# Kernel optimization log

Measured on AMD Instinct MI355X. Metric: run time of the kernel, lower is better.

## Reference

```python
import jax, jax.numpy as jnp
import numpy as np
import math

GOLDEN_CENTER = 1.0 / math.e
GOLDEN_LOWER = 0.5 - math.log(4.0 / 3.0)
GOLDEN_UPPER = 0.5

B, T, D = 4, 2048, 1024
E = 8
I = 4096 // (E // 2)  # expert_inter = 1024


def setup_inputs() -> dict:
    key = jax.random.key(0)
    k = jax.random.split(key, 6)
    s_d = 1.0 / math.sqrt(D)
    s_i = 1.0 / math.sqrt(I)
    return {
        "x": jax.random.normal(k[0], (B, T, D), jnp.float32),
        "Wg": jax.random.normal(k[1], (E, D, I), jnp.float32) * s_d,
        "Wu": jax.random.normal(k[2], (E, D, I), jnp.float32) * s_d,
        "Wd": jax.random.normal(k[3], (E, I, D), jnp.float32) * s_i,
        "Wr": jax.random.normal(k[4], (D, E), jnp.float32) * s_d,
        "temperature": jnp.ones((1,), jnp.float32),
    }


def _routing_weights(x, Wr, temperature):
    # inhibition: [B,T,E]
    inh = jax.nn.sigmoid((x @ Wr) / temperature)
    in_zone = (inh >= GOLDEN_LOWER) & (inh <= GOLDEN_UPPER)
    dist = jnp.abs(inh - GOLDEN_CENTER)
    w = jnp.exp(-dist / 0.1) * in_zone.astype(x.dtype)
    wsum = w.sum(axis=-1, keepdims=True)
    no_expert = wsum < 1e-8
    # fallback: softer decay, keep top-2 experts, renormalize
    fb = jnp.exp(-dist / 0.3)
    _, top2 = jax.lax.top_k(fb, 2)  # [B,T,2]
    fb_mask = jax.nn.one_hot(top2, E, dtype=x.dtype).sum(axis=-2)  # [B,T,E]
    fb_w = fb * fb_mask
    fb_w = fb_w / jnp.clip(fb_w.sum(axis=-1, keepdims=True), 1e-8)
    w = jnp.where(no_expert, fb_w, w)
    wsum = w.sum(axis=-1, keepdims=True)
    return w / jnp.clip(wsum, 1e-8)


def reference(x, Wg, Wu, Wd, Wr, temperature):
    weights = _routing_weights(x, Wr, temperature)  # [B,T,E]
    gate = jnp.einsum("btd,edi->beti", x, Wg)
    up = jnp.einsum("btd,edi->beti", x, Wu)
    h = jax.nn.silu(gate) * up  # [B,E,T,I]
    e_out = jnp.einsum("beti,eid->betd", h, Wd)
    out = jnp.einsum("bte,betd->btd", weights, e_out)
    return out
```

## Files before the change

kernel.cpp:

```cpp
#include <hip/hip_runtime.h>
#include <hip/hip_bf16.h>
#include <cstdint>

typedef __attribute__((ext_vector_type(8))) _Float16 f16x8;
typedef __attribute__((ext_vector_type(4))) _Float16 f16x4;
typedef __attribute__((ext_vector_type(4))) float f32x4;

#define GOLDEN_CENTER_F 0.36787944117144233f
#define GOLDEN_LOWER_F  0.21231792754821915f
#define GOLDEN_UPPER_F  0.5f

static constexpr int Dm = 1024;
static constexpr int Im = 1024;
static constexpr int NTOK = 8192;
static constexpr int NE = 8;

__device__ __forceinline__ void async16(const _Float16* g, _Float16* l) {
  __builtin_amdgcn_global_load_lds(
      (const __attribute__((address_space(1))) void*)g,
      (__attribute__((address_space(3))) void*)l,
      16, 0, 0);
}

__global__ void routing_kernel(const float* __restrict__ x, const float* __restrict__ Wr,
                               const float* __restrict__ temp, float* __restrict__ wts) {
  const int wave = threadIdx.x >> 6, lane = threadIdx.x & 63;
  const int t = blockIdx.x * 4 + wave;
  const float* xr = x + (size_t)t * Dm;
  float acc[NE] = {0.f,0.f,0.f,0.f,0.f,0.f,0.f,0.f};
  for (int d = lane; d < Dm; d += 64) {
    float xv = xr[d];
    const float* wr = Wr + (size_t)d * NE;
#pragma unroll
    for (int e = 0; e < NE; ++e) acc[e] += xv * wr[e];
  }
#pragma unroll
  for (int off = 32; off > 0; off >>= 1) {
#pragma unroll
    for (int e = 0; e < NE; ++e) acc[e] += __shfl_down(acc[e], off, 64);
  }
  if (lane == 0) {
    float T = temp[0];
    float w[NE], dist[NE];
    float wsum = 0.f;
#pragma unroll
    for (int e = 0; e < NE; ++e) {
      float inh = 1.f / (1.f + expf(-acc[e] / T));
      dist[e] = fabsf(inh - GOLDEN_CENTER_F);
      bool zone = (inh >= GOLDEN_LOWER_F) && (inh <= GOLDEN_UPPER_F);
      w[e] = zone ? expf(-dist[e] / 0.1f) : 0.f;
      wsum += w[e];
    }
    if (wsum < 1e-8f) {
      float fb[NE];
#pragma unroll
      for (int e = 0; e < NE; ++e) fb[e] = expf(-dist[e] / 0.3f);
      int i1 = 0;
      for (int e = 1; e < NE; ++e) if (fb[e] > fb[i1]) i1 = e;
      int i2 = (i1 == 0) ? 1 : 0;
      for (int e = 0; e < NE; ++e) if (e != i1 && fb[e] > fb[i2]) i2 = e;
      float s = fmaxf(fb[i1] + fb[i2], 1e-8f);
#pragma unroll
      for (int e = 0; e < NE; ++e) w[e] = 0.f;
      w[i1] = fb[i1] / s;
      w[i2] = fb[i2] / s;
      wsum = w[i1] + w[i2];
    }
    float inv = 1.f / fmaxf(wsum, 1e-8f);
#pragma unroll
    for (int e = 0; e < NE; ++e) wts[(size_t)t * NE + e] = w[e] * inv;
  }
}

__global__ void compact_kernel(const float* __restrict__ wts, int* __restrict__ tok,
                               float* __restrict__ wc, int* __restrict__ cnt,
                               int* __restrict__ pos) {
  const int e = blockIdx.x;
  const int tid = threadIdx.x;
  const int wave = tid >> 6, lane = tid & 63;
  __shared__ int wcnt[4];
  __shared__ int s_running;
  if (tid == 0) s_running = 0;
  __syncthreads();
  for (int base = 0; base < NTOK; base += 256) {
    int t = base + tid;
    float w = wts[(size_t)t * NE + e];
    bool act = w > 0.f;
    unsigned long long mask = __ballot(act);
    int prefix = __popcll(mask & ((1ull << lane) - 1ull));
    if (lane == 0) wcnt[wave] = __popcll(mask);
    __syncthreads();
    int wbase = 0;
    for (int i = 0; i < wave; ++i) wbase += wcnt[i];
    int run = s_running;
    int p = run + wbase + prefix;
    pos[(size_t)t * NE + e] = act ? p : -1;
    if (act) {
      tok[(size_t)e * NTOK + p] = t;
      wc[(size_t)e * NTOK + p] = w;
    }
    __syncthreads();
    if (tid == 0) s_running = run + wcnt[0] + wcnt[1] + wcnt[2] + wcnt[3];
    __syncthreads();
  }
  int c = s_running;
  if (tid == 0) cnt[e] = c;
  int padded = (c + 127) & ~127;
  for (int p = c + tid; p < padded; p += 256) {
    tok[(size_t)e * NTOK + p] = 0;
    wc[(size_t)e * NTOK + p] = 0.f;
  }
}

__global__ void cvt_x_kernel(const float* __restrict__ x, _Float16* __restrict__ xb) {
  size_t i = ((size_t)blockIdx.x * 256 + threadIdx.x) * 4;
  float4 v = *(const float4*)(x + i);
  f16x4 o = {(_Float16)v.x, (_Float16)v.y, (_Float16)v.z, (_Float16)v.w};
  *(f16x4*)(xb + i) = o;
}

__global__ void transpose_cvt_kernel(const float* __restrict__ Wg, const float* __restrict__ Wu,
                                     const float* __restrict__ Wd, _Float16* __restrict__ WgT,
                                     _Float16* __restrict__ WuT, _Float16* __restrict__ WdT) {
  __shared__ float tile[32][33];
  const int which = blockIdx.z >> 3;
  const int e = blockIdx.z & 7;
  const float* src = which == 0 ? Wg : which == 1 ? Wu : Wd;
  _Float16* dst = which == 0 ? WgT : which == 1 ? WuT : WdT;
  const size_t base = (size_t)e * 1024 * 1024;
  const int r0 = blockIdx.y * 32, c0 = blockIdx.x * 32;
  const int tx = threadIdx.x & 31, ty = threadIdx.x >> 5;
#pragma unroll
  for (int j = 0; j < 32; j += 8)
    tile[ty + j][tx] = src[base + (size_t)(r0 + ty + j) * 1024 + c0 + tx];
  __syncthreads();
#pragma unroll
  for (int j = 0; j < 32; j += 8)
    dst[base + (size_t)(c0 + ty + j) * 1024 + r0 + tx] = (_Float16)tile[tx][ty + j];
}

__global__ __launch_bounds__(256, 2) void gemm1_kernel(
    const _Float16* __restrict__ A, const _Float16* __restrict__ BgAll,
    const _Float16* __restrict__ BuAll, const int* __restrict__ tok,
    const int* __restrict__ cnt, _Float16* __restrict__ hbuf, int ebase) {
  constexpr int K = Dm;
  const int z = blockIdx.z;
  const int e = ebase + z;
  const int r0 = blockIdx.x * 128;
  if (r0 >= cnt[e]) return;
  const int n0 = blockIdx.y * 128;
  const _Float16* Bg = BgAll + (size_t)e * Dm * Im;
  const _Float16* Bu = BuAll + (size_t)e * Dm * Im;
  _Float16* H = hbuf + (size_t)z * NTOK * Im;
  const int* tk = tok + (size_t)e * NTOK;

  __shared__ _Float16 As[128 * 32];
  __shared__ _Float16 Bgs[128 * 32];
  __shared__ _Float16 Bus[128 * 32];
  const int tid = threadIdx.x;
  const int wave = tid >> 6, lane = tid & 63;
  const int m_off = (wave & 1) * 64, n_off = (wave >> 1) * 64;

  f32x4 accg[4][4], accu[4][4];
#pragma unroll
  for (int i = 0; i < 4; ++i)
#pragma unroll
    for (int j = 0; j < 4; ++j) { accg[i][j] = (f32x4)0.f; accu[i][j] = (f32x4)0.f; }

  const int srow = lane >> 2;
  const int scol = ((lane & 3) ^ ((srow >> 1) & 3)) * 8;
  const int ridx = r0 + wave * 32 + srow;
  const int tA0 = tk[ridx];
  const int tA1 = tk[ridx + 16];
  const _Float16* gA0 = A + (size_t)tA0 * K + scol;
  const _Float16* gA1 = A + (size_t)tA1 * K + scol;
  const _Float16* gBg = Bg + (size_t)(n0 + wave * 32 + srow) * K + scol;
  const _Float16* gBu = Bu + (size_t)(n0 + wave * 32 + srow) * K + scol;
  _Float16* lA  = As  + (wave * 32) * 32;
  _Float16* lBg = Bgs + (wave * 32) * 32;
  _Float16* lBu = Bus + (wave * 32) * 32;

  const int fr = lane & 15, fq = lane >> 4;
  const int sw = (fq ^ ((fr >> 1) & 3)) * 8;
  const int aoff = (m_off + fr) * 32 + sw;
  const int boff = (n_off + fr) * 32 + sw;

  for (int k0 = 0; k0 < K; k0 += 32) {
    __syncthreads();
    async16(gA0 + k0, lA);
    async16(gA1 + k0, lA + 16 * 32);
    async16(gBg + k0, lBg);
    async16(gBg + k0 + 16 * K, lBg + 16 * 32);
    async16(gBu + k0, lBu);
    async16(gBu + k0 + 16 * K, lBu + 16 * 32);
    __syncthreads();

    f16x8 af[4], bgf[4], buf2[4];
#pragma unroll
    for (int i = 0; i < 4; ++i) {
      af[i]   = *(const f16x8*)(As  + aoff + i * 16 * 32);
      bgf[i]  = *(const f16x8*)(Bgs + boff + i * 16 * 32);
      buf2[i] = *(const f16x8*)(Bus + boff + i * 16 * 32);
    }
#pragma unroll
    for (int im = 0; im < 4; ++im)
#pragma unroll
      for (int in2 = 0; in2 < 4; ++in2) {
        accg[im][in2] = __builtin_amdgcn_mfma_f32_16x16x32_f16(af[im], bgf[in2], accg[im][in2], 0, 0, 0);
        accu[im][in2] = __builtin_amdgcn_mfma_f32_16x16x32_f16(af[im], buf2[in2], accu[im][in2], 0, 0, 0);
      }
  }

#pragma unroll
  for (int im = 0; im < 4; ++im)
#pragma unroll
    for (int in2 = 0; in2 < 4; ++in2)
#pragma unroll
      for (int r = 0; r < 4; ++r) {
        int row = r0 + m_off + im * 16 + fq * 4 + r;
        int c = n0 + n_off + in2 * 16 + fr;
        float g = accg[im][in2][r], u = accu[im][in2][r];
        float s = g / (1.f + __expf(-g));
        H[(size_t)row * Im + c] = (_Float16)(s * u);
      }
}

__global__ __launch_bounds__(256, 2) void gemm2_kernel(
    const _Float16* __restrict__ hbuf, const _Float16* __restrict__ BAll,
    const int* __restrict__ cnt, _Float16* __restrict__ ebuf, int ebase) {
  constexpr int K = Im;
  const int z = blockIdx.z;
  const int e = ebase + z;
  const int r0 = blockIdx.x * 128;
  if (r0 >= cnt[e]) return;
  const int n0 = blockIdx.y * 128;
  const _Float16* A = hbuf + (size_t)z * NTOK * Im;
  const _Float16* B = BAll + (size_t)e * Im * Dm;
  _Float16* Ez = ebuf + (size_t)z * NTOK * Dm;

  __shared__ _Float16 As[128 * 32];
  __shared__ _Float16 Bs[128 * 32];
  const int tid = threadIdx.x;
  const int wave = tid >> 6, lane = tid & 63;
  const int m_off = (wave & 1) * 64, n_off = (wave >> 1) * 64;

  f32x4 acc[4][4];
#pragma unroll
  for (int i = 0; i < 4; ++i)
#pragma unroll
    for (int j = 0; j < 4; ++j) acc[i][j] = (f32x4)0.f;

  const int srow = lane >> 2;
  const int scol = ((lane & 3) ^ ((srow >> 1) & 3)) * 8;
  const _Float16* gA = A + (size_t)(r0 + wave * 32 + srow) * K + scol;
  const _Float16* gB = B + (size_t)(n0 + wave * 32 + srow) * K + scol;
  _Float16* lA = As + (wave * 32) * 32;
  _Float16* lB = Bs + (wave * 32) * 32;

  const int fr = lane & 15, fq = lane >> 4;
  const int sw = (fq ^ ((fr >> 1) & 3)) * 8;
  const int aoff = (m_off + fr) * 32 + sw;
  const int boff = (n_off + fr) * 32 + sw;

  for (int k0 = 0; k0 < K; k0 += 32) {
    __syncthreads();
    async16(gA + k0, lA);
    async16(gA + k0 + 16 * K, lA + 16 * 32);
    async16(gB + k0, lB);
    async16(gB + k0 + 16 * K, lB + 16 * 32);
    __syncthreads();

    f16x8 af[4], bf[4];
#pragma unroll
    for (int i = 0; i < 4; ++i) {
      af[i] = *(const f16x8*)(As + aoff + i * 16 * 32);
      bf[i] = *(const f16x8*)(Bs + boff + i * 16 * 32);
    }
#pragma unroll
    for (int im = 0; im < 4; ++im)
#pragma unroll
      for (int in2 = 0; in2 < 4; ++in2)
        acc[im][in2] = __builtin_amdgcn_mfma_f32_16x16x32_f16(af[im], bf[in2], acc[im][in2], 0, 0, 0);
  }

#pragma unroll
  for (int im = 0; im < 4; ++im)
#pragma unroll
    for (int in2 = 0; in2 < 4; ++in2)
#pragma unroll
      for (int r = 0; r < 4; ++r) {
        int row = m_off + im * 16 + fq * 4 + r;
        int c = n0 + n_off + in2 * 16 + fr;
        Ez[((size_t)(r0 + row)) * Dm + c] = (_Float16)acc[im][in2][r];
      }
}

__global__ void combine_kernel(const _Float16* __restrict__ ebuf, const int* __restrict__ pos,
                               const float* __restrict__ wts, float* __restrict__ out,
                               int ebase, int g, int accum) {
  const int t = blockIdx.x;
  __shared__ int sp[NE];
  __shared__ float sw[NE];
  if (threadIdx.x < g) {
    sp[threadIdx.x] = pos[(size_t)t * NE + ebase + threadIdx.x];
    sw[threadIdx.x] = wts[(size_t)t * NE + ebase + threadIdx.x];
  }
  __syncthreads();
  const int c = threadIdx.x * 4;
  float4 s;
  if (accum) s = *(const float4*)(out + (size_t)t * Dm + c);
  else s = float4{0.f, 0.f, 0.f, 0.f};
  for (int j = 0; j < g; ++j) {
    int p = sp[j];
    if (p >= 0) {
      float w = sw[j];
      f16x4 v = *(const f16x4*)(ebuf + ((size_t)j * NTOK + p) * Dm + c);
      s.x += w * (float)v[0];
      s.y += w * (float)v[1];
      s.z += w * (float)v[2];
      s.w += w * (float)v[3];
    }
  }
  *(float4*)(out + (size_t)t * Dm + c) = s;
}

extern "C" void kernel_launch(void* const* d_in, const int* in_sizes, int n_in,
                              void* d_out, int out_size, void* d_ws, size_t ws_size,
                              hipStream_t stream) {
  const float* x    = (const float*)d_in[0];
  const float* Wg   = (const float*)d_in[1];
  const float* Wu   = (const float*)d_in[2];
  const float* Wd   = (const float*)d_in[3];
  const float* Wr   = (const float*)d_in[4];
  const float* temp = (const float*)d_in[5];
  float* out = (float*)d_out;

  char* ws = (char*)d_ws;
  size_t off = 0;
  auto carve = [&](size_t bytes) {
    char* p = ws + off;
    off = (off + bytes + 255) & ~(size_t)255;
    return p;
  };
  float* wts = (float*)carve((size_t)NTOK * NE * 4);
  int*   tok = (int*)  carve((size_t)NE * NTOK * 4);
  float* wc  = (float*)carve((size_t)NE * NTOK * 4);
  int*   pos = (int*)  carve((size_t)NTOK * NE * 4);
  int*   cnt = (int*)  carve(4096);
  _Float16* xb   = (_Float16*)carve((size_t)NTOK * Dm * 2);
  _Float16* WgT  = (_Float16*)carve((size_t)NE * Dm * Im * 2);
  _Float16* WuT  = (_Float16*)carve((size_t)NE * Dm * Im * 2);
  _Float16* WdT  = (_Float16*)carve((size_t)NE * Dm * Im * 2);
  const size_t fixed_off = off;
  const size_t per_expert = (size_t)NTOK * Im * 2 + (size_t)NTOK * Dm * 2;
  int g = (ws_size >= fixed_off + 8 * per_expert) ? 8 : 4;
  _Float16* hbuf = (_Float16*)carve((size_t)g * NTOK * Im * 2);
  _Float16* ebuf = (_Float16*)carve((size_t)g * NTOK * Dm * 2);

  routing_kernel<<<NTOK / 4, 256, 0, stream>>>(x, Wr, temp, wts);
  compact_kernel<<<NE, 256, 0, stream>>>(wts, tok, wc, cnt, pos);
  cvt_x_kernel<<<(NTOK * Dm) / 1024, 256, 0, stream>>>(x, xb);
  transpose_cvt_kernel<<<dim3(32, 32, 24), 256, 0, stream>>>(Wg, Wu, Wd, WgT, WuT, WdT);

  for (int e0 = 0; e0 < NE; e0 += g) {
    gemm1_kernel<<<dim3(NTOK / 128, Im / 128, g), 256, 0, stream>>>(xb, WgT, WuT, tok, cnt, hbuf, e0);
    gemm2_kernel<<<dim3(NTOK / 128, Dm / 128, g), 256, 0, stream>>>(hbuf, WdT, cnt, ebuf, e0);
    combine_kernel<<<NTOK, 256, 0, stream>>>(ebuf, pos, wts, out, e0, g, e0 > 0);
  }
}
```

Baseline: 487.7 us.

## Double-buffer GEMM K-loop with 64-wide tiles and interleave gate/up weights

Both expert GEMMs now use double-buffered LDS tiles of K=64, issuing async loads for the next tile before computing the current one and waiting with explicit vmcnt counters instead of two full barriers per step. Gate and up weights are packed into one interleaved [2048 x D] matrix so gemm1 runs as a single GEMM whose adjacent 16-column blocks pair gate and up for the SiLU epilogue. The fp16 conversion of x is folded into the routing kernel, removing a separate launch and a second read of x. LDS use per block rises to 64KB, which may limit occupancy.

```diff
diff --git a/kernel.cpp b/kernel.cpp
--- a/kernel.cpp
+++ b/kernel.cpp
@@ -23,16 +23,23 @@
 }
 
 __global__ void routing_kernel(const float* __restrict__ x, const float* __restrict__ Wr,
-                               const float* __restrict__ temp, float* __restrict__ wts) {
+                               const float* __restrict__ temp, float* __restrict__ wts,
+                               _Float16* __restrict__ xb) {
   const int wave = threadIdx.x >> 6, lane = threadIdx.x & 63;
   const int t = blockIdx.x * 4 + wave;
   const float* xr = x + (size_t)t * Dm;
+  _Float16* xo = xb + (size_t)t * Dm;
   float acc[NE] = {0.f,0.f,0.f,0.f,0.f,0.f,0.f,0.f};
-  for (int d = lane; d < Dm; d += 64) {
-    float xv = xr[d];
-    const float* wr = Wr + (size_t)d * NE;
-#pragma unroll
-    for (int e = 0; e < NE; ++e) acc[e] += xv * wr[e];
+  const int d0 = lane * 16;
+#pragma unroll
+  for (int j = 0; j < 4; ++j) {
+    float4 v = *(const float4*)(xr + d0 + j * 4);
+    f16x4 h = {(_Float16)v.x, (_Float16)v.y, (_Float16)v.z, (_Float16)v.w};
+    *(f16x4*)(xo + d0 + j * 4) = h;
+    const float* wr = Wr + (size_t)(d0 + j * 4) * NE;
+#pragma unroll
+    for (int e = 0; e < NE; ++e)
+      acc[e] += v.x * wr[e] + v.y * wr[NE + e] + v.z * wr[2 * NE + e] + v.w * wr[3 * NE + e];
   }
 #pragma unroll
   for (int off = 32; off > 0; off >>= 1) {
@@ -112,137 +119,170 @@
   }
 }
 
-__global__ void cvt_x_kernel(const float* __restrict__ x, _Float16* __restrict__ xb) {
-  size_t i = ((size_t)blockIdx.x * 256 + threadIdx.x) * 4;
-  float4 v = *(const float4*)(x + i);
-  f16x4 o = {(_Float16)v.x, (_Float16)v.y, (_Float16)v.z, (_Float16)v.w};
-  *(f16x4*)(xb + i) = o;
-}
-
 __global__ void transpose_cvt_kernel(const float* __restrict__ Wg, const float* __restrict__ Wu,
-                                     const float* __restrict__ Wd, _Float16* __restrict__ WgT,
-                                     _Float16* __restrict__ WuT, _Float16* __restrict__ WdT) {
+                                     const float* __restrict__ Wd, _Float16* __restrict__ Wgu,
+                                     _Float16* __restrict__ WdT) {
   __shared__ float tile[32][33];
   const int which = blockIdx.z >> 3;
   const int e = blockIdx.z & 7;
   const float* src = which == 0 ? Wg : which == 1 ? Wu : Wd;
-  _Float16* dst = which == 0 ? WgT : which == 1 ? WuT : WdT;
-  const size_t base = (size_t)e * 1024 * 1024;
+  const size_t sbase = (size_t)e * 1024 * 1024;
   const int r0 = blockIdx.y * 32, c0 = blockIdx.x * 32;
   const int tx = threadIdx.x & 31, ty = threadIdx.x >> 5;
 #pragma unroll
   for (int j = 0; j < 32; j += 8)
-    tile[ty + j][tx] = src[base + (size_t)(r0 + ty + j) * 1024 + c0 + tx];
+    tile[ty + j][tx] = src[sbase + (size_t)(r0 + ty + j) * 1024 + c0 + tx];
   __syncthreads();
 #pragma unroll
-  for (int j = 0; j < 32; j += 8)
-    dst[base + (size_t)(c0 + ty + j) * 1024 + r0 + tx] = (_Float16)tile[tx][ty + j];
-}
+  for (int j = 0; j < 32; j += 8) {
+    const int c = c0 + ty + j;
+    float v = tile[tx][ty + j];
+    if (which == 2) {
+      WdT[sbase + (size_t)c * 1024 + r0 + tx] = (_Float16)v;
+    } else {
+      const int n = ((c >> 4) << 5) + (which << 4) + (c & 15);
+      Wgu[(size_t)e * 2048 * 1024 + (size_t)n * 1024 + r0 + tx] = (_Float16)v;
+    }
+  }
+}
+
 
 __global__ __launch_bounds__(256, 2) void gemm1_kernel(
-    const _Float16* __restrict__ A, const _Float16* __restrict__ BgAll,
-    const _Float16* __restrict__ BuAll, const int* __restrict__ tok,
-    const int* __restrict__ cnt, _Float16* __restrict__ hbuf, int ebase) {
-  constexpr int K = Dm;
+    const _Float16* __restrict__ A, const _Float16* __restrict__ Bgu,
+    const int* __restrict__ tok, const int* __restrict__ cnt,
+    _Float16* __restrict__ hbuf, int ebase) {
+  constexpr int K = Dm, NT = K / 64;
   const int z = blockIdx.z;
   const int e = ebase + z;
   const int r0 = blockIdx.x * 128;
   if (r0 >= cnt[e]) return;
   const int n0 = blockIdx.y * 128;
-  const _Float16* Bg = BgAll + (size_t)e * Dm * Im;
-  const _Float16* Bu = BuAll + (size_t)e * Dm * Im;
+  const _Float16* Bm = Bgu + (size_t)e * 2048 * Dm;
   _Float16* H = hbuf + (size_t)z * NTOK * Im;
   const int* tk = tok + (size_t)e * NTOK;
 
-  __shared__ _Float16 As[128 * 32];
-  __shared__ _Float16 Bgs[128 * 32];
-  __shared__ _Float16 Bus[128 * 32];
-  const int tid = threadIdx.x;
-  const int wave = tid >> 6, lane = tid & 63;
-  const int m_off = (wave & 1) * 64, n_off = (wave >> 1) * 64;
-
-  f32x4 accg[4][4], accu[4][4];
+  __shared__ _Float16 sA[2][8192];
+  __shared__ _Float16 sB[2][8192];
+  const int tid = threadIdx.x, lane = tid & 63, w = tid >> 6;
+  const int m_off = (w & 1) * 64, n_off = (w >> 1) * 64;
+
+  const int lcc = (tid & 7) ^ ((tid >> 3) & 7);
+  const _Float16* pA[4];
+  const _Float16* pB[4];
+#pragma unroll
+  for (int j = 0; j < 4; ++j) {
+    pA[j] = A + (size_t)tk[r0 + j * 32 + (tid >> 3)] * K + lcc * 8;
+    pB[j] = Bm + (size_t)(n0 + j * 32 + (tid >> 3)) * K + lcc * 8;
+  }
+
+  auto STAGE = [&](int b, int ko) {
+#pragma unroll
+    for (int j = 0; j < 4; ++j) async16(pA[j] + ko, &sA[b][(j * 256 + tid) * 8]);
+#pragma unroll
+    for (int j = 0; j < 4; ++j) async16(pB[j] + ko, &sB[b][(j * 256 + tid) * 8]);
+  };
+
+  const int fr = lane & 15, fq = lane >> 4;
+  const int axr = (m_off + fr) * 64;
+  const int bxr = (n_off + fr) * 64;
+  const int c0 = (fq ^ (fr & 7)) * 8;
+  const int c1 = ((4 + fq) ^ (fr & 7)) * 8;
+
+  f32x4 acc[4][4];
 #pragma unroll
   for (int i = 0; i < 4; ++i)
 #pragma unroll
-    for (int j = 0; j < 4; ++j) { accg[i][j] = (f32x4)0.f; accu[i][j] = (f32x4)0.f; }
-
-  const int srow = lane >> 2;
-  const int scol = ((lane & 3) ^ ((srow >> 1) & 3)) * 8;
-  const int ridx = r0 + wave * 32 + srow;
-  const int tA0 = tk[ridx];
-  const int tA1 = tk[ridx + 16];
-  const _Float16* gA0 = A + (size_t)tA0 * K + scol;
-  const _Float16* gA1 = A + (size_t)tA1 * K + scol;
-  const _Float16* gBg = Bg + (size_t)(n0 + wave * 32 + srow) * K + scol;
-  const _Float16* gBu = Bu + (size_t)(n0 + wave * 32 + srow) * K + scol;
-  _Float16* lA  = As  + (wave * 32) * 32;
-  _Float16* lBg = Bgs + (wave * 32) * 32;
-  _Float16* lBu = Bus + (wave * 32) * 32;
-
-  const int fr = lane & 15, fq = lane >> 4;
-  const int sw = (fq ^ ((fr >> 1) & 3)) * 8;
-  const int aoff = (m_off + fr) * 32 + sw;
-  const int boff = (n_off + fr) * 32 + sw;
-
-  for (int k0 = 0; k0 < K; k0 += 32) {
-    __syncthreads();
-    async16(gA0 + k0, lA);
-    async16(gA1 + k0, lA + 16 * 32);
-    async16(gBg + k0, lBg);
-    async16(gBg + k0 + 16 * K, lBg + 16 * 32);
-    async16(gBu + k0, lBu);
-    async16(gBu + k0 + 16 * K, lBu + 16 * 32);
-    __syncthreads();
-
-    f16x8 af[4], bgf[4], buf2[4];
-#pragma unroll
-    for (int i = 0; i < 4; ++i) {
-      af[i]   = *(const f16x8*)(As  + aoff + i * 16 * 32);
-      bgf[i]  = *(const f16x8*)(Bgs + boff + i * 16 * 32);
-      buf2[i] = *(const f16x8*)(Bus + boff + i * 16 * 32);
-    }
+    for (int j = 0; j < 4; ++j) acc[i][j] = (f32x4)0.f;
+
+  STAGE(0, 0);
+  for (int t = 0; t < NT; ++t) {
+    const int p = t & 1;
+    if (t + 1 < NT) {
+      STAGE(p ^ 1, (t + 1) * 64);
+      asm volatile("s_waitcnt vmcnt(8)\n\ts_barrier" ::: "memory");
+    } else {
+      asm volatile("s_waitcnt vmcnt(0)\n\ts_barrier" ::: "memory");
+    }
+    const _Float16* Ab = sA[p];
+    const _Float16* Bb = sB[p];
+    f16x8 af[4], bf[4];
+#pragma unroll
+    for (int i = 0; i < 4; ++i) af[i] = *(const f16x8*)(Ab + axr + i * 1024 + c0);
+#pragma unroll
+    for (int i = 0; i < 4; ++i) bf[i] = *(const f16x8*)(Bb + bxr + i * 1024 + c0);
 #pragma unroll
     for (int im = 0; im < 4; ++im)
 #pragma unroll
-      for (int in2 = 0; in2 < 4; ++in2) {
-        accg[im][in2] = __builtin_amdgcn_mfma_f32_16x16x32_f16(af[im], bgf[in2], accg[im][in2], 0, 0, 0);
-        accu[im][in2] = __builtin_amdgcn_mfma_f32_16x16x32_f16(af[im], buf2[in2], accu[im][in2], 0, 0, 0);
+      for (int in = 0; in < 4; ++in)
+        acc[im][in] = __builtin_amdgcn_mfma_f32_16x16x32_f16(af[im], bf[in], acc[im][in], 0, 0, 0);
+#pragma unroll
+    for (int i = 0; i < 4; ++i) af[i] = *(const f16x8*)(Ab + axr + i * 1024 + c1);
+#pragma unroll
+    for (int i = 0; i < 4; ++i) bf[i] = *(const f16x8*)(Bb + bxr + i * 1024 + c1);
+#pragma unroll
+    for (int im = 0; im < 4; ++im)
+#pragma unroll
+      for (int in = 0; in < 4; ++in)
+        acc[im][in] = __builtin_amdgcn_mfma_f32_16x16x32_f16(af[im], bf[in], acc[im][in], 0, 0, 0);
+    asm volatile("s_waitcnt lgkmcnt(0)\n\ts_barrier" ::: "memory");
+  }
+
+  const int hc0 = ((n0 + n_off) >> 1) + fr;
+#pragma unroll
+  for (int im = 0; im < 4; ++im) {
+    const int rowb = r0 + m_off + im * 16 + fq * 4;
+#pragma unroll
+    for (int q = 0; q < 2; ++q) {
+      const int hcol = hc0 + q * 16;
+#pragma unroll
+      for (int r = 0; r < 4; ++r) {
+        float g = acc[im][2 * q][r], u = acc[im][2 * q + 1][r];
+        float s = g / (1.f + __expf(-g));
+        H[(size_t)(rowb + r) * Im + hcol] = (_Float16)(s * u);
       }
-  }
-
-#pragma unroll
-  for (int im = 0; im < 4; ++im)
-#pragma unroll
-    for (int in2 = 0; in2 < 4; ++in2)
-#pragma unroll
-      for (int r = 0; r < 4; ++r) {
-        int row = r0 + m_off + im * 16 + fq * 4 + r;
-        int c = n0 + n_off + in2 * 16 + fr;
-        float g = accg[im][in2][r], u = accu[im][in2][r];
-        float s = g / (1.f + __expf(-g));
-        H[(size_t)row * Im + c] = (_Float16)(s * u);
-      }
+    }
+  }
 }
 
 __global__ __launch_bounds__(256, 2) void gemm2_kernel(
-    const _Float16* __restrict__ hbuf, const _Float16* __restrict__ BAll,
+    const _Float16* __restrict__ hb, const _Float16* __restrict__ BAll,
     const int* __restrict__ cnt, _Float16* __restrict__ ebuf, int ebase) {
-  constexpr int K = Im;
+  constexpr int K = Im, NT = K / 64;
   const int z = blockIdx.z;
   const int e = ebase + z;
   const int r0 = blockIdx.x * 128;
   if (r0 >= cnt[e]) return;
   const int n0 = blockIdx.y * 128;
-  const _Float16* A = hbuf + (size_t)z * NTOK * Im;
-  const _Float16* B = BAll + (size_t)e * Im * Dm;
+  const _Float16* A = hb + (size_t)z * NTOK * Im;
+  const _Float16* Bm = BAll + (size_t)e * Im * Dm;
   _Float16* Ez = ebuf + (size_t)z * NTOK * Dm;
 
-  __shared__ _Float16 As[128 * 32];
-  __shared__ _Float16 Bs[128 * 32];
-  const int tid = threadIdx.x;
-  const int wave = tid >> 6, lane = tid & 63;
-  const int m_off = (wave & 1) * 64, n_off = (wave >> 1) * 64;
+  __shared__ _Float16 sA[2][8192];
+  __shared__ _Float16 sB[2][8192];
+  const int tid = threadIdx.x, lane = tid & 63, w = tid >> 6;
+  const int m_off = (w & 1) * 64, n_off = (w >> 1) * 64;
+
+  const int lcc = (tid & 7) ^ ((tid >> 3) & 7);
+  const _Float16* pA[4];
+  const _Float16* pB[4];
+#pragma unroll
+  for (int j = 0; j < 4; ++j) {
+    pA[j] = A + (size_t)(r0 + j * 32 + (tid >> 3)) * K + lcc * 8;
+    pB[j] = Bm + (size_t)(n0 + j * 32 + (tid >> 3)) * K + lcc * 8;
+  }
+
+  auto STAGE = [&](int b, int ko) {
+#pragma unroll
+    for (int j = 0; j < 4; ++j) async16(pA[j] + ko, &sA[b][(j * 256 + tid) * 8]);
+#pragma unroll
+    for (int j = 0; j < 4; ++j) async16(pB[j] + ko, &sB[b][(j * 256 + tid) * 8]);
+  };
+
+  const int fr = lane & 15, fq = lane >> 4;
+  const int axr = (m_off + fr) * 64;
+  const int bxr = (n_off + fr) * 64;
+  const int c0 = (fq ^ (fr & 7)) * 8;
+  const int c1 = ((4 + fq) ^ (fr & 7)) * 8;
 
   f32x4 acc[4][4];
 #pragma unroll
@@ -250,49 +290,50 @@
 #pragma unroll
     for (int j = 0; j < 4; ++j) acc[i][j] = (f32x4)0.f;
 
-  const int srow = lane >> 2;
-  const int scol = ((lane & 3) ^ ((srow >> 1) & 3)) * 8;
-  const _Float16* gA = A + (size_t)(r0 + wave * 32 + srow) * K + scol;
-  const _Float16* gB = B + (size_t)(n0 + wave * 32 + srow) * K + scol;
-  _Float16* lA = As + (wave * 32) * 32;
-  _Float16* lB = Bs + (wave * 32) * 32;
-
-  const int fr = lane & 15, fq = lane >> 4;
-  const int sw = (fq ^ ((fr >> 1) & 3)) * 8;
-  const int aoff = (m_off + fr) * 32 + sw;
-  const int boff = (n_off + fr) * 32 + sw;
-
-  for (int k0 = 0; k0 < K; k0 += 32) {
-    __syncthreads();
-    async16(gA + k0, lA);
-    async16(gA + k0 + 16 * K, lA + 16 * 32);
-    async16(gB + k0, lB);
-    async16(gB + k0 + 16 * K, lB + 16 * 32);
-    __syncthreads();
-
+  STAGE(0, 0);
+  for (int t = 0; t < NT; ++t) {
+    const int p = t & 1;
+    if (t + 1 < NT) {
+      STAGE(p ^ 1, (t + 1) * 64);
+      asm volatile("s_waitcnt vmcnt(8)\n\ts_barrier" ::: "memory");
+    } else {
+      asm volatile("s_waitcnt vmcnt(0)\n\ts_barrier" ::: "memory");
+    }
+    const _Float16* Ab = sA[p];
+    const _Float16* Bb = sB[p];
     f16x8 af[4], bf[4];
 #pragma unroll
-    for (int i = 0; i < 4; ++i) {
-      af[i] = *(const f16x8*)(As + aoff + i * 16 * 32);
-      bf[i] = *(const f16x8*)(Bs + boff + i * 16 * 32);
-    }
+    for (int i = 0; i < 4; ++i) af[i] = *(const f16x8*)(Ab + axr + i * 1024 + c0);
+#pragma unroll
+    for (int i = 0; i < 4; ++i) bf[i] = *(const f16x8*)(Bb + bxr + i * 1024 + c0);
 #pragma unroll
     for (int im = 0; im < 4; ++im)
 #pragma unroll
-      for (int in2 = 0; in2 < 4; ++in2)
-        acc[im][in2] = __builtin_amdgcn_mfma_f32_16x16x32_f16(af[im], bf[in2], acc[im][in2], 0, 0, 0);
-  }
-
-#pragma unroll
-  for (int im = 0; im < 4; ++im)
-#pragma unroll
-    for (int in2 = 0; in2 < 4; ++in2)
-#pragma unroll
-      for (int r = 0; r < 4; ++r) {
-        int row = m_off + im * 16 + fq * 4 + r;
-        int c = n0 + n_off + in2 * 16 + fr;
-        Ez[((size_t)(r0 + row)) * Dm + c] = (_Float16)acc[im][in2][r];
-      }
+      for (int in = 0; in < 4; ++in)
+        acc[im][in] = __builtin_amdgcn_mfma_f32_16x16x32_f16(af[im], bf[in], acc[im][in], 0, 0, 0);
+#pragma unroll
+    for (int i = 0; i < 4; ++i) af[i] = *(const f16x8*)(Ab + axr + i * 1024 + c1);
+#pragma unroll
+    for (int i = 0; i < 4; ++i) bf[i] = *(const f16x8*)(Bb + bxr + i * 1024 + c1);
+#pragma unroll
+    for (int im = 0; im < 4; ++im)
+#pragma unroll
+      for (int in = 0; in < 4; ++in)
+        acc[im][in] = __builtin_amdgcn_mfma_f32_16x16x32_f16(af[im], bf[in], acc[im][in], 0, 0, 0);
+    asm volatile("s_waitcnt lgkmcnt(0)\n\ts_barrier" ::: "memory");
+  }
+
+#pragma unroll
+  for (int im = 0; im < 4; ++im) {
+    const int rowb = r0 + m_off + im * 16 + fq * 4;
+#pragma unroll
+    for (int in = 0; in < 4; ++in) {
+      const int col = n0 + n_off + in * 16 + fr;
+#pragma unroll
+      for (int r = 0; r < 4; ++r)
+        Ez[(size_t)(rowb + r) * Dm + col] = (_Float16)acc[im][in][r];
+    }
+  }
 }
 
 __global__ void combine_kernel(const _Float16* __restrict__ ebuf, const int* __restrict__ pos,
@@ -300,10 +341,10 @@
                                int ebase, int g, int accum) {
   const int t = blockIdx.x;
   __shared__ int sp[NE];
-  __shared__ float sw[NE];
+  __shared__ float swt[NE];
   if (threadIdx.x < g) {
     sp[threadIdx.x] = pos[(size_t)t * NE + ebase + threadIdx.x];
-    sw[threadIdx.x] = wts[(size_t)t * NE + ebase + threadIdx.x];
+    swt[threadIdx.x] = wts[(size_t)t * NE + ebase + threadIdx.x];
   }
   __syncthreads();
   const int c = threadIdx.x * 4;
@@ -313,7 +354,7 @@
   for (int j = 0; j < g; ++j) {
     int p = sp[j];
     if (p >= 0) {
-      float w = sw[j];
+      float w = swt[j];
       f16x4 v = *(const f16x4*)(ebuf + ((size_t)j * NTOK + p) * Dm + c);
       s.x += w * (float)v[0];
       s.y += w * (float)v[1];
@@ -348,22 +389,20 @@
   int*   pos = (int*)  carve((size_t)NTOK * NE * 4);
   int*   cnt = (int*)  carve(4096);
   _Float16* xb   = (_Float16*)carve((size_t)NTOK * Dm * 2);
-  _Float16* WgT  = (_Float16*)carve((size_t)NE * Dm * Im * 2);
-  _Float16* WuT  = (_Float16*)carve((size_t)NE * Dm * Im * 2);
-  _Float16* WdT  = (_Float16*)carve((size_t)NE * Dm * Im * 2);
+  _Float16* Wgu  = (_Float16*)carve((size_t)NE * 2048 * Dm * 2);
+  _Float16* WdT  = (_Float16*)carve((size_t)NE * Im * Dm * 2);
   const size_t fixed_off = off;
   const size_t per_expert = (size_t)NTOK * Im * 2 + (size_t)NTOK * Dm * 2;
   int g = (ws_size >= fixed_off + 8 * per_expert) ? 8 : 4;
   _Float16* hbuf = (_Float16*)carve((size_t)g * NTOK * Im * 2);
   _Float16* ebuf = (_Float16*)carve((size_t)g * NTOK * Dm * 2);
 
-  routing_kernel<<<NTOK / 4, 256, 0, stream>>>(x, Wr, temp, wts);
+  routing_kernel<<<NTOK / 4, 256, 0, stream>>>(x, Wr, temp, wts, xb);
   compact_kernel<<<NE, 256, 0, stream>>>(wts, tok, wc, cnt, pos);
-  cvt_x_kernel<<<(NTOK * Dm) / 1024, 256, 0, stream>>>(x, xb);
-  transpose_cvt_kernel<<<dim3(32, 32, 24), 256, 0, stream>>>(Wg, Wu, Wd, WgT, WuT, WdT);
+  transpose_cvt_kernel<<<dim3(32, 32, 24), 256, 0, stream>>>(Wg, Wu, Wd, Wgu, WdT);
 
   for (int e0 = 0; e0 < NE; e0 += g) {
-    gemm1_kernel<<<dim3(NTOK / 128, Im / 128, g), 256, 0, stream>>>(xb, WgT, WuT, tok, cnt, hbuf, e0);
+    gemm1_kernel<<<dim3(NTOK / 128, 2048 / 128, g), 256, 0, stream>>>(xb, Wgu, tok, cnt, hbuf, e0);
     gemm2_kernel<<<dim3(NTOK / 128, Dm / 128, g), 256, 0, stream>>>(hbuf, WdT, cnt, ebuf, e0);
     combine_kernel<<<NTOK, 256, 0, stream>>>(ebuf, pos, wts, out, e0, g, e0 > 0);
   }
```

Result: no change. 487.8 us (+0.0%).
